# Performance work log

Measured on AMD Instinct MI355X. Metric: run time of the kernel, lower is better.

The kernel has to match this reference:

```python
import jax, jax.numpy as jnp
import numpy as np

BS, D, M = 64, 256, 512


def setup_inputs() -> dict:
    key = jax.random.key(0)
    ks = jax.random.split(key, 6)
    # Small scales keep the 10-step RLS recurrence numerically stable.
    A_start = 0.05 * jax.random.normal(ks[0], (BS, D, D), dtype=jnp.float32)
    Y1 = 0.05 * jax.random.normal(ks[1], (BS, D, M), dtype=jnp.float32)
    Y2 = 0.05 * jax.random.normal(ks[2], (BS, D, M), dtype=jnp.float32)
    y1 = 0.05 * jax.random.normal(ks[3], (BS, D, 1), dtype=jnp.float32)
    y2 = 0.05 * jax.random.normal(ks[4], (BS, D, 1), dtype=jnp.float32)
    eye = jnp.broadcast_to(jnp.eye(D, dtype=jnp.float32), (BS, D, D))
    P_inv_start = 1e-3 * eye + 1e-4 * jax.random.normal(ks[5], (BS, D, D), dtype=jnp.float32)
    return {"A_start": A_start, "Y1": Y1, "Y2": Y2, "y1": y1, "y2": y2,
            "P_inv_start": P_inv_start, "h": 2, "m_prox": 10}


def _t(x):
    return jnp.swapaxes(x, 1, 2)


def reference(A_start, Y1, Y2, y1, y2, P_inv_start, h, m_prox):
    """Faithful jax version of DelayedDMD.update.

    The torch code recomputes `A_t + P_inv @ (Y1 @ (Y2^T - Y1^T @ A_t))` twice
    per step; here it is computed once (same math, fused).
    """
    Y1t, Y2t, y1t, y2t = _t(Y1), _t(Y2), _t(y1), _t(y2)
    denom = 1.0 + y1t @ P_inv_start @ y1          # (bs, 1, 1)
    Piy1 = P_inv_start @ y1                       # (bs, d, 1)

    def step(A_t, _):
        # batch recursive-least-squares prox iteration
        M_ = A_t + P_inv_start @ (Y1 @ (Y2t - Y1t @ A_t))   # (bs, d, d)
        A_new = M_ + y1 @ (y2t - y1t @ M_) / denom
        return A_new, None

    A_final_t, _ = jax.lax.scan(step, _t(A_start), None, length=m_prox)
    P_inv_new = P_inv_start - Piy1 @ (y1t @ P_inv_start) / denom
    return _t(A_final_t), P_inv_new
```

## Files before the change

### kernel.cpp

```cpp
#include <hip/hip_runtime.h>
#include <hip/hip_bf16.h>
#include <stdint.h>


#define BSZ 64
#define DD 256
#define MM 512

typedef __attribute__((ext_vector_type(8))) short short8;
typedef __attribute__((ext_vector_type(4))) float f32x4;

__device__ __forceinline__ unsigned short f2b(float f) {
    unsigned int u = __float_as_uint(f);
    unsigned int r = (u + 0x7fffu + ((u >> 16) & 1u)) >> 16;
    return (unsigned short)r;
}
__device__ __forceinline__ float b2f(unsigned short s) {
    return __uint_as_float(((unsigned int)s) << 16);
}


__global__ __launch_bounds__(256)
void prep1(const float* __restrict__ P, const float* __restrict__ y1g,
           unsigned short* __restrict__ Pb, float* __restrict__ vec,
           float* __restrict__ qpart)
{
    const int blk = blockIdx.x, t = threadIdx.x;
    const int b = blk >> 2, rs = (blk & 3) * 64;
    const long base = (long)b * DD * DD;
    const int wv = t >> 6, ln = t & 63;
    __shared__ float sy1[DD];
    __shared__ float qsh[4][DD];
    sy1[t] = y1g[b * DD + t];
    __syncthreads();
    const int col4 = ln * 4;
    const float4 yv = *(const float4*)(sy1 + col4);
    float ql0 = 0.f, ql1 = 0.f, ql2 = 0.f, ql3 = 0.f;
#pragma unroll
    for (int i = 0; i < 16; ++i) {
        const int row = rs + i * 4 + wv;
        const long o = base + (long)row * DD + col4;
        float4 p = *(const float4*)(P + o);
        ushort4 u;
        u.x = f2b(p.x); u.y = f2b(p.y); u.z = f2b(p.z); u.w = f2b(p.w);
        *(ushort4*)(Pb + o) = u;
        const float yr = sy1[row];
        ql0 += yr * p.x; ql1 += yr * p.y; ql2 += yr * p.z; ql3 += yr * p.w;
        float s = p.x * yv.x + p.y * yv.y + p.z * yv.z + p.w * yv.w;
#pragma unroll
        for (int off = 32; off; off >>= 1) s += __shfl_down(s, off, 64);
        if (ln == 0) vec[(long)b * 768 + row] = s;
    }
    *(float4*)(qsh[wv] + col4) = make_float4(ql0, ql1, ql2, ql3);
    __syncthreads();
    qpart[((long)blk) * DD + t] = qsh[0][t] + qsh[1][t] + qsh[2][t] + qsh[3][t];
}

__global__ __launch_bounds__(256)
void prep2(const float* __restrict__ Y1, const float* __restrict__ Y2,
           const float* __restrict__ y1g, const float* __restrict__ qpart,
           unsigned short* __restrict__ G1b, unsigned short* __restrict__ G21b,
           float* __restrict__ vec)
{
    __shared__ __align__(16) unsigned short As[128 * 32];
    __shared__ __align__(16) unsigned short Bs[128 * 32];
    const int blk = blockIdx.x, t = threadIdx.x;
    if (blk < 512) {
        const int quad = blk & 3, z = blk >> 2, sel = z >> 6, b = z & 63;
        const int i0 = (quad >> 1) * 128, j0 = (quad & 1) * 128;
        const float* Af = (sel ? Y2 : Y1) + (long)b * DD * MM;
        const float* Bf = Y1 + (long)b * DD * MM;
        unsigned short* Ob = (sel ? G21b : G1b) + (long)b * DD * DD;
        const int wv = t >> 6, ln = t & 63;
        const int lr = ln & 15, qd = ln >> 4;
        const int mh = (wv >> 1) * 64, nh = (wv & 1) * 64;
        const int srow = t >> 3, sk4 = (t & 7) * 4;
        f32x4 acc[4][4] = {};
        for (int kc = 0; kc < MM; kc += 32) {
#pragma unroll
            for (int i = 0; i < 4; ++i) {
                const int row = i * 32 + srow;
                float4 a = *(const float4*)(Af + (long)(i0 + row) * MM + kc + sk4);
                float4 c = *(const float4*)(Bf + (long)(j0 + row) * MM + kc + sk4);
                ushort4 ua, uc;
                ua.x = f2b(a.x); ua.y = f2b(a.y); ua.z = f2b(a.z); ua.w = f2b(a.w);
                uc.x = f2b(c.x); uc.y = f2b(c.y); uc.z = f2b(c.z); uc.w = f2b(c.w);
                *(ushort4*)(As + row * 32 + sk4) = ua;
                *(ushort4*)(Bs + row * 32 + sk4) = uc;
            }
            __syncthreads();
            short8 af[4], bfr[4];
#pragma unroll
            for (int mt = 0; mt < 4; ++mt)
                af[mt] = *(const short8*)(As + (mh + mt * 16 + lr) * 32 + qd * 8);
#pragma unroll
            for (int nt = 0; nt < 4; ++nt)
                bfr[nt] = *(const short8*)(Bs + (nh + nt * 16 + lr) * 32 + qd * 8);
#pragma unroll
            for (int mt = 0; mt < 4; ++mt)
#pragma unroll
                for (int nt = 0; nt < 4; ++nt)
                    acc[mt][nt] = __builtin_amdgcn_mfma_f32_16x16x32_bf16(
                        af[mt], bfr[nt], acc[mt][nt], 0, 0, 0);
            __syncthreads();
        }
#pragma unroll
        for (int mt = 0; mt < 4; ++mt)
#pragma unroll
            for (int nt = 0; nt < 4; ++nt) {
                const int gr0 = i0 + mh + mt * 16 + qd * 4;
                const int gc  = j0 + nh + nt * 16 + lr;
#pragma unroll
                for (int r = 0; r < 4; ++r)
                    Ob[(long)(gr0 + r) * DD + gc] = f2b(acc[mt][nt][r]);
            }
        return;
    }
    const int b = blk - 512;
    float* vb = vec + (long)b * 768;
    const float* qp = qpart + (long)b * 4 * DD;
    vb[256 + t] = qp[t] + qp[DD + t] + qp[2 * DD + t] + qp[3 * DD + t];
    __shared__ float red[256];
    red[t] = vb[t] * y1g[b * DD + t];
    __syncthreads();
    for (int s = 128; s; s >>= 1) { if (t < s) red[t] += red[t + s]; __syncthreads(); }
    if (t == 0) vb[512] = 1.0f / (1.0f + red[0]);
}

__global__ __launch_bounds__(256)
void gemmEV(const unsigned short* __restrict__ Pb, const unsigned short* __restrict__ G1b,
            const unsigned short* __restrict__ G21b,
            const float* __restrict__ P,
            const float* __restrict__ y1g, const float* __restrict__ y2g,
            const float* __restrict__ vec,
            unsigned short* __restrict__ Enb, unsigned short* __restrict__ Vpb,
            float* __restrict__ out2)
{
    __shared__ __align__(16) unsigned short As[128 * 32];
    __shared__ __align__(16) unsigned short Bs[128 * 32];
    __shared__ float qs[DD], s1[DD], s2[DD];
    const int blk = blockIdx.x, t = threadIdx.x;
    if (blk >= 512) {
        const int c = blk - 512, b = c >> 2, rs = (c & 3) * 64;
        const long base = (long)b * DD * DD;
        const float* vb = vec + (long)b * 768;
        const float kk = vb[512];
#pragma unroll 4
        for (int i = 0; i < 16; ++i) {
            const int idx = rs * DD + (i * 256 + t) * 4;
            const int row = idx >> 8, col = idx & 255;
            const float kPi = kk * vb[row];
            float4 p = *(const float4*)(P + base + idx);
            float4 q = *(const float4*)(vb + 256 + col);
            float4 rr;
            rr.x = p.x - kPi * q.x; rr.y = p.y - kPi * q.y;
            rr.z = p.z - kPi * q.z; rr.w = p.w - kPi * q.w;
            *(float4*)(out2 + base + idx) = rr;
        }
        return;
    }
    const int quad = blk & 3, z = blk >> 2, sel = z >> 6, b = z & 63;
    const int i0 = (quad >> 1) * 128, j0 = (quad & 1) * 128;
    const unsigned short* Ab = (sel ? G21b : Pb) + (long)b * DD * DD;
    const unsigned short* Bb = (sel ? Pb : G1b) + (long)b * DD * DD;
    unsigned short* Ob = (sel ? Vpb : Enb) + (long)b * DD * DD;
    const float* vb = vec + (long)b * 768;
    const int wv = t >> 6, ln = t & 63;
    const int lr = ln & 15, qd = ln >> 4;
    const int mh = (wv >> 1) * 64, nh = (wv & 1) * 64;
    const int srow = t >> 3, sk4 = (t & 7) * 4;

    qs[t] = vb[256 + t];
    s1[t] = y1g[b * DD + t];
    s2[t] = y2g[b * DD + t];

    f32x4 acc[4][4] = {};
    float dot[4] = {0.f, 0.f, 0.f, 0.f};

    for (int kc = 0; kc < DD; kc += 32) {
#pragma unroll
        for (int i = 0; i < 4; ++i) {
            const int row = i * 32 + srow;
            *(ushort4*)(As + row * 32 + sk4) =
                *(const ushort4*)(Ab + (long)(i0 + row) * DD + kc + sk4);
            *(ushort4*)(Bs + row * 32 + sk4) =
                *(const ushort4*)(Bb + (long)(j0 + row) * DD + kc + sk4);
        }
        __syncthreads();
        short8 af[4], bfr[4];
#pragma unroll
        for (int mt = 0; mt < 4; ++mt)
            af[mt] = *(const short8*)(As + (mh + mt * 16 + lr) * 32 + qd * 8);
#pragma unroll
        for (int nt = 0; nt < 4; ++nt)
            bfr[nt] = *(const short8*)(Bs + (nh + nt * 16 + lr) * 32 + qd * 8);
        const float4 qa = *(const float4*)(qs + kc + qd * 8);
        const float4 qb = *(const float4*)(qs + kc + qd * 8 + 4);
        const float qf[8] = {qa.x, qa.y, qa.z, qa.w, qb.x, qb.y, qb.z, qb.w};
        if (!sel) {
#pragma unroll
            for (int nt = 0; nt < 4; ++nt)
#pragma unroll
                for (int j = 0; j < 8; ++j)
                    dot[nt] += b2f((unsigned short)bfr[nt][j]) * qf[j];
        } else {
#pragma unroll
            for (int mt = 0; mt < 4; ++mt)
#pragma unroll
                for (int j = 0; j < 8; ++j)
                    dot[mt] += b2f((unsigned short)af[mt][j]) * qf[j];
        }
#pragma unroll
        for (int mt = 0; mt < 4; ++mt)
#pragma unroll
            for (int nt = 0; nt < 4; ++nt)
                acc[mt][nt] = __builtin_amdgcn_mfma_f32_16x16x32_bf16(
                    af[mt], bfr[nt], acc[mt][nt], 0, 0, 0);
        __syncthreads();
    }
#pragma unroll
    for (int i = 0; i < 4; ++i) {
        dot[i] += __shfl_xor(dot[i], 16, 64);
        dot[i] += __shfl_xor(dot[i], 32, 64);
    }
    const float kk = vb[512];
#pragma unroll
    for (int mt = 0; mt < 4; ++mt) {
#pragma unroll
        for (int nt = 0; nt < 4; ++nt) {
            const int gr0 = i0 + mh + mt * 16 + qd * 4;
            const int gc  = j0 + nh + nt * 16 + lr;
            if (!sel) {
                const float cw = s1[gc] - dot[nt];
#pragma unroll
                for (int r = 0; r < 4; ++r) {
                    const float rv = kk * s1[gr0 + r];
                    Ob[(long)(gr0 + r) * DD + gc] = f2b(-(acc[mt][nt][r] + rv * cw));
                }
            } else {
                const float cv = s1[gc];
#pragma unroll
                for (int r = 0; r < 4; ++r) {
                    const float uv = __shfl(dot[mt], qd * 4 + r, 64);
                    const float rv = kk * (s2[gr0 + r] - uv);
                    Ob[(long)(gr0 + r) * DD + gc] = f2b(acc[mt][nt][r] + rv * cv);
                }
            }
        }
    }
}

#define SWZ(row) (((row) ^ ((row) >> 3)) & 7)
__global__ __launch_bounds__(256, 2)
void iterk(const float* __restrict__ A_start, const unsigned short* __restrict__ Enb,
           const unsigned short* __restrict__ Vpb, float* __restrict__ out1)
{
    __shared__ __align__(16) unsigned short Ash[32 * 256];
    const int b = blockIdx.y, r0 = blockIdx.x * 32;
    const long base = (long)b * DD * DD;
    const float* Ab = A_start + base;
    const unsigned short* Eb = Enb + base;
    const unsigned short* Vb = Vpb + base;
    float* Ob = out1 + base;
    const int t = threadIdx.x, wv = t >> 6, ln = t & 63;
    const int lr = ln & 15, qd = ln >> 4;

    f32x4 acc[2][4], vv[2][4];
    short8 ef[4][8];

#pragma unroll
    for (int mt = 0; mt < 2; ++mt)
#pragma unroll
        for (int j = 0; j < 4; ++j) {
            const int col = wv * 64 + j * 16 + lr;
            const int rowb = r0 + mt * 16 + qd * 4;
#pragma unroll
            for (int r = 0; r < 4; ++r) {
                const long o = (long)(rowb + r) * DD + col;
                acc[mt][j][r] = Ab[o];
                vv[mt][j][r]  = b2f(Vb[o]);
            }
        }
#pragma unroll
    for (int j = 0; j < 4; ++j) {
        const int n = wv * 64 + j * 16 + lr;
#pragma unroll
        for (int kc = 0; kc < 8; ++kc)
            ef[j][kc] = *(const short8*)(Eb + (long)n * DD + kc * 32 + qd * 8);
    }

#pragma unroll 1
    for (int s = 0; s < 10; ++s) {
        const int cgb = wv * 8 + (lr >> 3), cb = lr & 7;
#pragma unroll
        for (int mt = 0; mt < 2; ++mt)
#pragma unroll
            for (int j = 0; j < 4; ++j) {
#pragma unroll
                for (int r = 0; r < 4; ++r) {
                    const int lrow = mt * 16 + qd * 4 + r;
                    const int cg = (cgb + j * 2) ^ SWZ(lrow);
                    Ash[lrow * 256 + cg * 8 + cb] = f2b(acc[mt][j][r]);
                }
                acc[mt][j] += vv[mt][j];
            }
        __syncthreads();
#pragma unroll
        for (int kc = 0; kc < 8; ++kc) {
            short8 af[2];
#pragma unroll
            for (int mt = 0; mt < 2; ++mt) {
                const int row = mt * 16 + lr;
                const int cg = (kc * 4 + qd) ^ SWZ(row);
                af[mt] = *(const short8*)(Ash + row * 256 + cg * 8);
            }
#pragma unroll
            for (int mt = 0; mt < 2; ++mt)
#pragma unroll
                for (int j = 0; j < 4; ++j)
                    acc[mt][j] = __builtin_amdgcn_mfma_f32_16x16x32_bf16(
                        af[mt], ef[j][kc], acc[mt][j], 0, 0, 0);
        }
        __syncthreads();
    }

#pragma unroll
    for (int mt = 0; mt < 2; ++mt)
#pragma unroll
        for (int j = 0; j < 4; ++j) {
            const int col = wv * 64 + j * 16 + lr;
            const int rowb = r0 + mt * 16 + qd * 4;
#pragma unroll
            for (int r = 0; r < 4; ++r)
                Ob[(long)(rowb + r) * DD + col] = acc[mt][j][r];
        }
}

extern "C" void kernel_launch(void* const* d_in, const int* in_sizes, int n_in,
                              void* d_out, int out_size, void* d_ws, size_t ws_size,
                              hipStream_t stream)
{
    const float* A_start = (const float*)d_in[0];
    const float* Y1      = (const float*)d_in[1];
    const float* Y2      = (const float*)d_in[2];
    const float* y1      = (const float*)d_in[3];
    const float* y2      = (const float*)d_in[4];
    const float* P       = (const float*)d_in[5];

    const long EL2 = (long)BSZ * DD * DD;

    float* out1 = (float*)d_out;
    float* out2 = out1 + EL2;

    char* w8 = (char*)d_ws;
    unsigned short* Pb    = (unsigned short*)(w8);
    unsigned short* G1b   = (unsigned short*)(w8 + 8388608);
    unsigned short* G21b  = (unsigned short*)(w8 + 16777216);
    unsigned short* Enb   = (unsigned short*)(w8 + 25165824);
    unsigned short* Vpb   = (unsigned short*)(w8 + 33554432);
    float*          vec   = (float*)(w8 + 41943040);
    float*          qpart = (float*)(w8 + 42139648);

    const dim3 blk(256);

    prep1<<<256, blk, 0, stream>>>(P, y1, Pb, vec, qpart);
    prep2<<<576, blk, 0, stream>>>(Y1, Y2, y1, qpart, G1b, G21b, vec);
    gemmEV<<<768, blk, 0, stream>>>(Pb, G1b, G21b, P, y1, y2, vec, Enb, Vpb, out2);
    iterk<<<dim3(8, 64), blk, 0, stream>>>(A_start, Enb, Vpb, out1);
}
```

Measured before the change: 212.3 us.

## Prefetch and swizzle GEMM tiles, widen K chunks, move P_inv update into iterk

The prep2 and gemmEV GEMM loops now use larger K chunks (64 and 128) held in XOR-swizzled LDS. The next chunk's global loads are issued into registers while MFMAs run on the current one. prep1 uses twice as many blocks with up-front loads, and the qpart reduction is adjusted to 8 partials. The P_inv_new elementwise update moves from gemmEV into extra blocks of iterk. These changes target exposed load latency, LDS bank conflicts and tail imbalance, at the cost of more registers and LDS per block, which may lower occupancy.

```diff
diff --git a/kernel.cpp b/kernel.cpp
--- a/kernel.cpp
+++ b/kernel.cpp
@@ -26,7 +26,7 @@
            float* __restrict__ qpart)
 {
     const int blk = blockIdx.x, t = threadIdx.x;
-    const int b = blk >> 2, rs = (blk & 3) * 64;
+    const int b = blk >> 3, rs = (blk & 7) * 32;
     const long base = (long)b * DD * DD;
     const int wv = t >> 6, ln = t & 63;
     __shared__ float sy1[DD];
@@ -35,12 +35,18 @@
     __syncthreads();
     const int col4 = ln * 4;
     const float4 yv = *(const float4*)(sy1 + col4);
+    float4 pr[8];
+#pragma unroll
+    for (int i = 0; i < 8; ++i) {
+        const int row = rs + i * 4 + wv;
+        pr[i] = *(const float4*)(P + base + (long)row * DD + col4);
+    }
     float ql0 = 0.f, ql1 = 0.f, ql2 = 0.f, ql3 = 0.f;
 #pragma unroll
-    for (int i = 0; i < 16; ++i) {
+    for (int i = 0; i < 8; ++i) {
         const int row = rs + i * 4 + wv;
         const long o = base + (long)row * DD + col4;
-        float4 p = *(const float4*)(P + o);
+        const float4 p = pr[i];
         ushort4 u;
         u.x = f2b(p.x); u.y = f2b(p.y); u.z = f2b(p.z); u.w = f2b(p.w);
         *(ushort4*)(Pb + o) = u;
@@ -62,8 +68,8 @@
            unsigned short* __restrict__ G1b, unsigned short* __restrict__ G21b,
            float* __restrict__ vec)
 {
-    __shared__ __align__(16) unsigned short As[128 * 32];
-    __shared__ __align__(16) unsigned short Bs[128 * 32];
+    __shared__ __align__(16) unsigned short As[128 * 64];
+    __shared__ __align__(16) unsigned short Bs[128 * 64];
     const int blk = blockIdx.x, t = threadIdx.x;
     if (blk < 512) {
         const int quad = blk & 3, z = blk >> 2, sel = z >> 6, b = z & 63;
@@ -74,36 +80,57 @@
         const int wv = t >> 6, ln = t & 63;
         const int lr = ln & 15, qd = ln >> 4;
         const int mh = (wv >> 1) * 64, nh = (wv & 1) * 64;
-        const int srow = t >> 3, sk4 = (t & 7) * 4;
+        const int srow = t >> 4, sc4 = t & 15;
         f32x4 acc[4][4] = {};
-        for (int kc = 0; kc < MM; kc += 32) {
-#pragma unroll
-            for (int i = 0; i < 4; ++i) {
-                const int row = i * 32 + srow;
-                float4 a = *(const float4*)(Af + (long)(i0 + row) * MM + kc + sk4);
-                float4 c = *(const float4*)(Bf + (long)(j0 + row) * MM + kc + sk4);
-                ushort4 ua, uc;
-                ua.x = f2b(a.x); ua.y = f2b(a.y); ua.z = f2b(a.z); ua.w = f2b(a.w);
-                uc.x = f2b(c.x); uc.y = f2b(c.y); uc.z = f2b(c.z); uc.w = f2b(c.w);
-                *(ushort4*)(As + row * 32 + sk4) = ua;
-                *(ushort4*)(Bs + row * 32 + sk4) = uc;
+        float4 fa[8], fb[8];
+
+#define PRE2_ISSUE(kc)                                                          \
+        _Pragma("unroll")                                                       \
+        for (int i = 0; i < 8; ++i) {                                           \
+            const int row = i * 16 + srow;                                      \
+            fa[i] = *(const float4*)(Af + (long)(i0 + row) * MM + (kc) * 64 + sc4 * 4); \
+            fb[i] = *(const float4*)(Bf + (long)(j0 + row) * MM + (kc) * 64 + sc4 * 4); \
+        }
+
+        PRE2_ISSUE(0);
+        for (int kc = 0; kc < 8; ++kc) {
+#pragma unroll
+            for (int i = 0; i < 8; ++i) {
+                const int row = i * 16 + srow;
+                const int cb = (sc4 * 8) ^ ((row & 7) << 4);
+                ushort4 ua, ub;
+                ua.x = f2b(fa[i].x); ua.y = f2b(fa[i].y); ua.z = f2b(fa[i].z); ua.w = f2b(fa[i].w);
+                ub.x = f2b(fb[i].x); ub.y = f2b(fb[i].y); ub.z = f2b(fb[i].z); ub.w = f2b(fb[i].w);
+                *(ushort4*)((char*)As + row * 128 + cb) = ua;
+                *(ushort4*)((char*)Bs + row * 128 + cb) = ub;
             }
             __syncthreads();
-            short8 af[4], bfr[4];
-#pragma unroll
-            for (int mt = 0; mt < 4; ++mt)
-                af[mt] = *(const short8*)(As + (mh + mt * 16 + lr) * 32 + qd * 8);
-#pragma unroll
-            for (int nt = 0; nt < 4; ++nt)
-                bfr[nt] = *(const short8*)(Bs + (nh + nt * 16 + lr) * 32 + qd * 8);
-#pragma unroll
-            for (int mt = 0; mt < 4; ++mt)
-#pragma unroll
-                for (int nt = 0; nt < 4; ++nt)
-                    acc[mt][nt] = __builtin_amdgcn_mfma_f32_16x16x32_bf16(
-                        af[mt], bfr[nt], acc[mt][nt], 0, 0, 0);
+            if (kc < 7) PRE2_ISSUE(kc + 1);
+#pragma unroll
+            for (int kc2 = 0; kc2 < 2; ++kc2) {
+                short8 af[4], bfr[4];
+#pragma unroll
+                for (int mt = 0; mt < 4; ++mt) {
+                    const int row = mh + mt * 16 + lr;
+                    af[mt] = *(const short8*)((char*)As + row * 128 +
+                                              ((kc2 * 64 + qd * 16) ^ ((row & 7) << 4)));
+                }
+#pragma unroll
+                for (int nt = 0; nt < 4; ++nt) {
+                    const int row = nh + nt * 16 + lr;
+                    bfr[nt] = *(const short8*)((char*)Bs + row * 128 +
+                                               ((kc2 * 64 + qd * 16) ^ ((row & 7) << 4)));
+                }
+#pragma unroll
+                for (int mt = 0; mt < 4; ++mt)
+#pragma unroll
+                    for (int nt = 0; nt < 4; ++nt)
+                        acc[mt][nt] = __builtin_amdgcn_mfma_f32_16x16x32_bf16(
+                            af[mt], bfr[nt], acc[mt][nt], 0, 0, 0);
+            }
             __syncthreads();
         }
+#undef PRE2_ISSUE
 #pragma unroll
         for (int mt = 0; mt < 4; ++mt)
 #pragma unroll
@@ -118,8 +145,11 @@
     }
     const int b = blk - 512;
     float* vb = vec + (long)b * 768;
-    const float* qp = qpart + (long)b * 4 * DD;
-    vb[256 + t] = qp[t] + qp[DD + t] + qp[2 * DD + t] + qp[3 * DD + t];
+    const float* qp = qpart + (long)b * 8 * DD;
+    float qv = 0.f;
+#pragma unroll
+    for (int c = 0; c < 8; ++c) qv += qp[c * DD + t];
+    vb[256 + t] = qv;
     __shared__ float red[256];
     red[t] = vb[t] * y1g[b * DD + t];
     __syncthreads();
@@ -130,15 +160,134 @@
 __global__ __launch_bounds__(256)
 void gemmEV(const unsigned short* __restrict__ Pb, const unsigned short* __restrict__ G1b,
             const unsigned short* __restrict__ G21b,
-            const float* __restrict__ P,
             const float* __restrict__ y1g, const float* __restrict__ y2g,
             const float* __restrict__ vec,
-            unsigned short* __restrict__ Enb, unsigned short* __restrict__ Vpb,
-            float* __restrict__ out2)
+            unsigned short* __restrict__ Enb, unsigned short* __restrict__ Vpb)
 {
-    __shared__ __align__(16) unsigned short As[128 * 32];
-    __shared__ __align__(16) unsigned short Bs[128 * 32];
+    __shared__ __align__(16) unsigned short As[128 * 128];
+    __shared__ __align__(16) unsigned short Bs[128 * 128];
     __shared__ float qs[DD], s1[DD], s2[DD];
+    const int blk = blockIdx.x, t = threadIdx.x;
+    const int quad = blk & 3, z = blk >> 2, sel = z >> 6, b = z & 63;
+    const int i0 = (quad >> 1) * 128, j0 = (quad & 1) * 128;
+    const unsigned short* Ab = (sel ? G21b : Pb) + (long)b * DD * DD;
+    const unsigned short* Bb = (sel ? Pb : G1b) + (long)b * DD * DD;
+    unsigned short* Ob = (sel ? Vpb : Enb) + (long)b * DD * DD;
+    const float* vb = vec + (long)b * 768;
+    const int wv = t >> 6, ln = t & 63;
+    const int lr = ln & 15, qd = ln >> 4;
+    const int mh = (wv >> 1) * 64, nh = (wv & 1) * 64;
+    const int srow = t >> 4, sc16 = t & 15;
+
+    qs[t] = vb[256 + t];
+    s1[t] = y1g[b * DD + t];
+    s2[t] = y2g[b * DD + t];
+
+    f32x4 acc[4][4] = {};
+    float dot[4] = {0.f, 0.f, 0.f, 0.f};
+    uint4 ra[8], rb[8];
+
+#define GEV_ISSUE(kc)                                                           \
+    _Pragma("unroll")                                                           \
+    for (int i = 0; i < 8; ++i) {                                               \
+        const int row = i * 16 + srow;                                          \
+        ra[i] = *(const uint4*)(Ab + (long)(i0 + row) * DD + (kc) * 128 + sc16 * 8); \
+        rb[i] = *(const uint4*)(Bb + (long)(j0 + row) * DD + (kc) * 128 + sc16 * 8); \
+    }
+
+    GEV_ISSUE(0);
+#pragma unroll
+    for (int kc = 0; kc < 2; ++kc) {
+#pragma unroll
+        for (int i = 0; i < 8; ++i) {
+            const int row = i * 16 + srow;
+            const int cb = (sc16 * 16) ^ ((row & 7) << 4);
+            *(uint4*)((char*)As + row * 256 + cb) = ra[i];
+            *(uint4*)((char*)Bs + row * 256 + cb) = rb[i];
+        }
+        __syncthreads();
+        if (kc == 0) GEV_ISSUE(1);
+#pragma unroll
+        for (int kc2 = 0; kc2 < 4; ++kc2) {
+            short8 af[4], bfr[4];
+#pragma unroll
+            for (int mt = 0; mt < 4; ++mt) {
+                const int row = mh + mt * 16 + lr;
+                af[mt] = *(const short8*)((char*)As + row * 256 +
+                                          ((kc2 * 64 + qd * 16) ^ ((row & 7) << 4)));
+            }
+#pragma unroll
+            for (int nt = 0; nt < 4; ++nt) {
+                const int row = nh + nt * 16 + lr;
+                bfr[nt] = *(const short8*)((char*)Bs + row * 256 +
+                                           ((kc2 * 64 + qd * 16) ^ ((row & 7) << 4)));
+            }
+            const int kb = kc * 128 + kc2 * 32;
+            const float4 qa = *(const float4*)(qs + kb + qd * 8);
+            const float4 qb = *(const float4*)(qs + kb + qd * 8 + 4);
+            const float qf[8] = {qa.x, qa.y, qa.z, qa.w, qb.x, qb.y, qb.z, qb.w};
+            if (!sel) {
+#pragma unroll
+                for (int nt = 0; nt < 4; ++nt)
+#pragma unroll
+                    for (int j = 0; j < 8; ++j)
+                        dot[nt] += b2f((unsigned short)bfr[nt][j]) * qf[j];
+            } else {
+#pragma unroll
+                for (int mt = 0; mt < 4; ++mt)
+#pragma unroll
+                    for (int j = 0; j < 8; ++j)
+                        dot[mt] += b2f((unsigned short)af[mt][j]) * qf[j];
+            }
+#pragma unroll
+            for (int mt = 0; mt < 4; ++mt)
+#pragma unroll
+                for (int nt = 0; nt < 4; ++nt)
+                    acc[mt][nt] = __builtin_amdgcn_mfma_f32_16x16x32_bf16(
+                        af[mt], bfr[nt], acc[mt][nt], 0, 0, 0);
+        }
+        __syncthreads();
+    }
+#undef GEV_ISSUE
+#pragma unroll
+    for (int i = 0; i < 4; ++i) {
+        dot[i] += __shfl_xor(dot[i], 16, 64);
+        dot[i] += __shfl_xor(dot[i], 32, 64);
+    }
+    const float kk = vb[512];
+#pragma unroll
+    for (int mt = 0; mt < 4; ++mt) {
+#pragma unroll
+        for (int nt = 0; nt < 4; ++nt) {
+            const int gr0 = i0 + mh + mt * 16 + qd * 4;
+            const int gc  = j0 + nh + nt * 16 + lr;
+            if (!sel) {
+                const float cw = s1[gc] - dot[nt];
+#pragma unroll
+                for (int r = 0; r < 4; ++r) {
+                    const float rv = kk * s1[gr0 + r];
+                    Ob[(long)(gr0 + r) * DD + gc] = f2b(-(acc[mt][nt][r] + rv * cw));
+                }
+            } else {
+                const float cv = s1[gc];
+#pragma unroll
+                for (int r = 0; r < 4; ++r) {
+                    const float uv = __shfl(dot[mt], qd * 4 + r, 64);
+                    const float rv = kk * (s2[gr0 + r] - uv);
+                    Ob[(long)(gr0 + r) * DD + gc] = f2b(acc[mt][nt][r] + rv * cv);
+                }
+            }
+        }
+    }
+}
+
+#define SWZ(row) (((row) ^ ((row) >> 3)) & 7)
+__global__ __launch_bounds__(256, 2)
+void iterk(const float* __restrict__ A_start, const unsigned short* __restrict__ Enb,
+           const unsigned short* __restrict__ Vpb,
+           const float* __restrict__ P, const float* __restrict__ vec,
+           float* __restrict__ out1, float* __restrict__ out2)
+{
     const int blk = blockIdx.x, t = threadIdx.x;
     if (blk >= 512) {
         const int c = blk - 512, b = c >> 2, rs = (c & 3) * 64;
@@ -159,110 +308,14 @@
         }
         return;
     }
-    const int quad = blk & 3, z = blk >> 2, sel = z >> 6, b = z & 63;
-    const int i0 = (quad >> 1) * 128, j0 = (quad & 1) * 128;
-    const unsigned short* Ab = (sel ? G21b : Pb) + (long)b * DD * DD;
-    const unsigned short* Bb = (sel ? Pb : G1b) + (long)b * DD * DD;
-    unsigned short* Ob = (sel ? Vpb : Enb) + (long)b * DD * DD;
-    const float* vb = vec + (long)b * 768;
-    const int wv = t >> 6, ln = t & 63;
-    const int lr = ln & 15, qd = ln >> 4;
-    const int mh = (wv >> 1) * 64, nh = (wv & 1) * 64;
-    const int srow = t >> 3, sk4 = (t & 7) * 4;
-
-    qs[t] = vb[256 + t];
-    s1[t] = y1g[b * DD + t];
-    s2[t] = y2g[b * DD + t];
-
-    f32x4 acc[4][4] = {};
-    float dot[4] = {0.f, 0.f, 0.f, 0.f};
-
-    for (int kc = 0; kc < DD; kc += 32) {
-#pragma unroll
-        for (int i = 0; i < 4; ++i) {
-            const int row = i * 32 + srow;
-            *(ushort4*)(As + row * 32 + sk4) =
-                *(const ushort4*)(Ab + (long)(i0 + row) * DD + kc + sk4);
-            *(ushort4*)(Bs + row * 32 + sk4) =
-                *(const ushort4*)(Bb + (long)(j0 + row) * DD + kc + sk4);
-        }
-        __syncthreads();
-        short8 af[4], bfr[4];
-#pragma unroll
-        for (int mt = 0; mt < 4; ++mt)
-            af[mt] = *(const short8*)(As + (mh + mt * 16 + lr) * 32 + qd * 8);
-#pragma unroll
-        for (int nt = 0; nt < 4; ++nt)
-            bfr[nt] = *(const short8*)(Bs + (nh + nt * 16 + lr) * 32 + qd * 8);
-        const float4 qa = *(const float4*)(qs + kc + qd * 8);
-        const float4 qb = *(const float4*)(qs + kc + qd * 8 + 4);
-        const float qf[8] = {qa.x, qa.y, qa.z, qa.w, qb.x, qb.y, qb.z, qb.w};
-        if (!sel) {
-#pragma unroll
-            for (int nt = 0; nt < 4; ++nt)
-#pragma unroll
-                for (int j = 0; j < 8; ++j)
-                    dot[nt] += b2f((unsigned short)bfr[nt][j]) * qf[j];
-        } else {
-#pragma unroll
-            for (int mt = 0; mt < 4; ++mt)
-#pragma unroll
-                for (int j = 0; j < 8; ++j)
-                    dot[mt] += b2f((unsigned short)af[mt][j]) * qf[j];
-        }
-#pragma unroll
-        for (int mt = 0; mt < 4; ++mt)
-#pragma unroll
-            for (int nt = 0; nt < 4; ++nt)
-                acc[mt][nt] = __builtin_amdgcn_mfma_f32_16x16x32_bf16(
-                    af[mt], bfr[nt], acc[mt][nt], 0, 0, 0);
-        __syncthreads();
-    }
-#pragma unroll
-    for (int i = 0; i < 4; ++i) {
-        dot[i] += __shfl_xor(dot[i], 16, 64);
-        dot[i] += __shfl_xor(dot[i], 32, 64);
-    }
-    const float kk = vb[512];
-#pragma unroll
-    for (int mt = 0; mt < 4; ++mt) {
-#pragma unroll
-        for (int nt = 0; nt < 4; ++nt) {
-            const int gr0 = i0 + mh + mt * 16 + qd * 4;
-            const int gc  = j0 + nh + nt * 16 + lr;
-            if (!sel) {
-                const float cw = s1[gc] - dot[nt];
-#pragma unroll
-                for (int r = 0; r < 4; ++r) {
-                    const float rv = kk * s1[gr0 + r];
-                    Ob[(long)(gr0 + r) * DD + gc] = f2b(-(acc[mt][nt][r] + rv * cw));
-                }
-            } else {
-                const float cv = s1[gc];
-#pragma unroll
-                for (int r = 0; r < 4; ++r) {
-                    const float uv = __shfl(dot[mt], qd * 4 + r, 64);
-                    const float rv = kk * (s2[gr0 + r] - uv);
-                    Ob[(long)(gr0 + r) * DD + gc] = f2b(acc[mt][nt][r] + rv * cv);
-                }
-            }
-        }
-    }
-}
-
-#define SWZ(row) (((row) ^ ((row) >> 3)) & 7)
-__global__ __launch_bounds__(256, 2)
-void iterk(const float* __restrict__ A_start, const unsigned short* __restrict__ Enb,
-           const unsigned short* __restrict__ Vpb, float* __restrict__ out1)
-{
     __shared__ __align__(16) unsigned short Ash[32 * 256];
-    const int b = blockIdx.y, r0 = blockIdx.x * 32;
+    const int b = blk >> 3, r0 = (blk & 7) * 32;
     const long base = (long)b * DD * DD;
     const float* Ab = A_start + base;
     const unsigned short* Eb = Enb + base;
     const unsigned short* Vb = Vpb + base;
     float* Ob = out1 + base;
-    const int t = threadIdx.x, wv = t >> 6, ln = t & 63;
+    const int wv = t >> 6, ln = t & 63;
     const int lr = ln & 15, qd = ln >> 4;
 
     f32x4 acc[2][4], vv[2][4];
@@ -363,8 +416,8 @@
 
     const dim3 blk(256);
 
-    prep1<<<256, blk, 0, stream>>>(P, y1, Pb, vec, qpart);
+    prep1<<<512, blk, 0, stream>>>(P, y1, Pb, vec, qpart);
     prep2<<<576, blk, 0, stream>>>(Y1, Y2, y1, qpart, G1b, G21b, vec);
-    gemmEV<<<768, blk, 0, stream>>>(Pb, G1b, G21b, P, y1, y2, vec, Enb, Vpb, out2);
-    iterk<<<dim3(8, 64), blk, 0, stream>>>(A_start, Enb, Vpb, out1);
-}
+    gemmEV<<<512, blk, 0, stream>>>(Pb, G1b, G21b, y1, y2, vec, Enb, Vpb);
+    iterk<<<768, blk, 0, stream>>>(A_start, Enb, Vpb, P, vec, out1, out2);
+}
```

After: 225.4 us. 6.2% more time.
